# Optimization experiments

Measured on AMD Instinct MI355X. Metric: run time of the kernel, lower is better.

Reference implementation:

```python
import jax, jax.numpy as jnp
import numpy as np

NODE_DIM = 32
NUM_NODES = 256
BATCH = 32
HIDDEN = 64


def setup_inputs() -> dict:
    key = jax.random.key(0)
    k1, k2, k3, k4, k5 = jax.random.split(key, 5)
    node_features = jax.random.normal(k1, (BATCH, NUM_NODES, NODE_DIM), dtype=jnp.float32)
    # nn.Linear(node_dim*2, 64): weight [64, 2*node_dim], bias [64]
    s1 = 1.0 / np.sqrt(2 * NODE_DIM)
    W1 = jax.random.uniform(k2, (HIDDEN, 2 * NODE_DIM), minval=-s1, maxval=s1, dtype=jnp.float32)
    b1 = jax.random.uniform(k3, (HIDDEN,), minval=-s1, maxval=s1, dtype=jnp.float32)
    # nn.Linear(64, 1): weight [1, 64], bias [1]
    s2 = 1.0 / np.sqrt(HIDDEN)
    W2 = jax.random.uniform(k4, (1, HIDDEN), minval=-s2, maxval=s2, dtype=jnp.float32)
    b2 = jax.random.uniform(k5, (1,), minval=-s2, maxval=s2, dtype=jnp.float32)
    return {"node_features": node_features, "W1": W1, "b1": b1, "W2": W2, "b2": b2}


def reference(node_features, W1, b1, W2, b2):
    # fc1(concat(x_i, x_j)) splits as x_i @ W1a^T + x_j @ W1b^T (exact same math,
    # avoids materializing the [B,N,N,2d] pair tensor).
    d = node_features.shape[-1]
    W1a, W1b = W1[:, :d], W1[:, d:]
    Ai = jnp.einsum('bnd,hd->bnh', node_features, W1a)  # [B,N,H]
    Aj = jnp.einsum('bnd,hd->bnh', node_features, W1b)  # [B,N,H]
    hidden = jax.nn.relu(Ai[:, :, None, :] + Aj[:, None, :, :] + b1)  # [B,N,N,H]
    logits = jnp.einsum('bijh,h->bij', hidden, W2[0]) + b2[0]  # [B,N,N]
    return jax.nn.sigmoid(logits)
```

## Files before the change

### kernel.cpp

```cpp
#include <hip/hip_runtime.h>

typedef _Float16 h2 __attribute__((ext_vector_type(2)));
typedef _Float16 h8 __attribute__((ext_vector_type(8)));

#define BB 32
#define NN 256
#define DD 32
#define HH 64
#define ET 64
#define XST 40
#define AST 72

#if defined(__has_builtin)
#  if __has_builtin(__builtin_amdgcn_fdot2)
#    define FDOT2(a, b, c) __builtin_amdgcn_fdot2((a), (b), (c), false)
#  endif
#endif
#ifndef FDOT2
#  define FDOT2(a, b, c) ((c) + (float)((a)[0]) * (float)((b)[0]) + (float)((a)[1]) * (float)((b)[1]))
#endif

__device__ __forceinline__ float sigmoidf_fast(float v) {
    return 1.0f / (1.0f + __expf(-v));
}

__global__ __launch_bounds__(256) void fused_kernel(const float* __restrict__ x, const float* __restrict__ W1,
                                                    const float* __restrict__ b1, const float* __restrict__ W2,
                                                    const float* __restrict__ b2, float* __restrict__ out)
{
    __shared__ _Float16 sX[128][XST];
    __shared__ _Float16 sW[128][XST];
    __shared__ _Float16 sAi[ET][AST];
    __shared__ _Float16 sAj[ET][AST];
    __shared__ _Float16 sW2h[HH];

    const int blk = blockIdx.x;
    const int jt = blk & 3;
    const int it = (blk >> 2) & 3;
    const int b  = blk >> 4;
    const int tid = threadIdx.x;

    for (int k = tid; k < HH * 2 * DD; k += 256) {
        int h = k >> 6, c = k & 63;
        int hc = (c < 32) ? h : h + 64;
        int d  = c & 31;
        int phys = (hc >> 3) + ((hc & 7) << 4);
        sW[phys][d] = (_Float16)W1[k];
    }
    const float* xb = x + (size_t)b * NN * DD;
    for (int k = tid; k < 128 * DD; k += 256) {
        int row = k >> 5, d = k & 31;
        int grow = (row < 64) ? (it * ET + row) : (jt * ET + (row - 64));
        int phys = (row & 64) + ((row & 63) >> 2) + ((row & 3) << 4);
        sX[phys][d] = (_Float16)xb[(size_t)grow * DD + d];
    }
    if (tid < HH) sW2h[tid] = (_Float16)W2[tid];
    __syncthreads();

    {
        const int tcol = tid & 15;
        const int trow = tid >> 4;
        const int side = tcol >> 3;
        const int xbase = side * 64 + trow;
        const int h0 = (tcol & 7) * 8;

        float pacc[4][8] = {};
#pragma unroll
        for (int ch = 0; ch < 4; ++ch) {
            h8 xv[4], wv[8];
#pragma unroll
            for (int rr = 0; rr < 4; ++rr)
                xv[rr] = *(const h8*)&sX[xbase + 16 * rr][ch * 8];
#pragma unroll
            for (int cc = 0; cc < 8; ++cc)
                wv[cc] = *(const h8*)&sW[tcol + 16 * cc][ch * 8];
#pragma unroll
            for (int rr = 0; rr < 4; ++rr)
#pragma unroll
                for (int cc = 0; cc < 8; ++cc) {
                    float a = pacc[rr][cc];
                    a = FDOT2(__builtin_shufflevector(xv[rr], xv[rr], 0, 1),
                              __builtin_shufflevector(wv[cc], wv[cc], 0, 1), a);
                    a = FDOT2(__builtin_shufflevector(xv[rr], xv[rr], 2, 3),
                              __builtin_shufflevector(wv[cc], wv[cc], 2, 3), a);
                    a = FDOT2(__builtin_shufflevector(xv[rr], xv[rr], 4, 5),
                              __builtin_shufflevector(wv[cc], wv[cc], 4, 5), a);
                    a = FDOT2(__builtin_shufflevector(xv[rr], xv[rr], 6, 7),
                              __builtin_shufflevector(wv[cc], wv[cc], 6, 7), a);
                    pacc[rr][cc] = a;
                }
        }
        float badd[8];
#pragma unroll
        for (int cc = 0; cc < 8; ++cc) badd[cc] = (side == 0) ? 0.f : b1[h0 + cc];
        _Float16* dst = (side == 0) ? &sAi[0][0] : &sAj[0][0];
#pragma unroll
        for (int rr = 0; rr < 4; ++rr) {
            h8 v;
#pragma unroll
            for (int q = 0; q < 8; ++q) v[q] = (_Float16)(pacc[rr][q] + badd[q]);
            *(h8*)&dst[(size_t)(4 * trow + rr) * AST + h0] = v;
        }
    }
    __syncthreads();

    const int jl = tid & 15;
    const int il = tid >> 4;
    h8 w2v[8];
#pragma unroll
    for (int q = 0; q < 8; ++q) w2v[q] = *(const h8*)&sW2h[q * 8];

    float eacc[4][4] = {};
#pragma unroll
    for (int c8 = 0; c8 < 8; ++c8) {
        h8 av[4], cv[4];
#pragma unroll
        for (int r = 0; r < 4; ++r) av[r] = *(const h8*)&sAi[il + 16 * r][c8 * 8];
#pragma unroll
        for (int c = 0; c < 4; ++c) cv[c] = *(const h8*)&sAj[jl + 16 * c][c8 * 8];
#pragma unroll
        for (int r = 0; r < 4; ++r)
#pragma unroll
            for (int c = 0; c < 4; ++c) {
                h8 z  = av[r] + cv[c];
                h8 rl = __builtin_elementwise_max(z, (h8)(_Float16)0);
                float a = eacc[r][c];
                a = FDOT2(__builtin_shufflevector(rl, rl, 0, 1), __builtin_shufflevector(w2v[c8], w2v[c8], 0, 1), a);
                a = FDOT2(__builtin_shufflevector(rl, rl, 2, 3), __builtin_shufflevector(w2v[c8], w2v[c8], 2, 3), a);
                a = FDOT2(__builtin_shufflevector(rl, rl, 4, 5), __builtin_shufflevector(w2v[c8], w2v[c8], 4, 5), a);
                a = FDOT2(__builtin_shufflevector(rl, rl, 6, 7), __builtin_shufflevector(w2v[c8], w2v[c8], 6, 7), a);
                eacc[r][c] = a;
            }
    }

    const float b2v = b2[0];
    size_t base = ((size_t)b * NN + (size_t)it * ET + il) * NN + (size_t)jt * ET + jl;
#pragma unroll
    for (int r = 0; r < 4; ++r)
#pragma unroll
        for (int c = 0; c < 4; ++c)
            out[base + (size_t)(16 * r) * NN + 16 * c] = sigmoidf_fast(eacc[r][c] + b2v);
}

extern "C" void kernel_launch(void* const* d_in, const int* in_sizes, int n_in,
                              void* d_out, int out_size, void* d_ws, size_t ws_size,
                              hipStream_t stream) {
    const float* x  = (const float*)d_in[0];
    const float* W1 = (const float*)d_in[1];
    const float* b1 = (const float*)d_in[2];
    const float* W2 = (const float*)d_in[3];
    const float* b2 = (const float*)d_in[4];
    float* out = (float*)d_out;

    const int nTiles = BB * (NN / ET) * (NN / ET);
    fused_kernel<<<nTiles, 256, 0, stream>>>(x, W1, b1, W2, b2, out);
}
```

Before: 19.14 us.

## Enlarge output tile to 128x64 per block and vectorize staging loads

Each block now computes a 128x64 output tile instead of 64x64, halving the block count to 256, so the per-block W1 conversion and Aj projection are amortized over twice as many outputs. The prologue loads W1 and x as float4 and writes h8 vectors to shared memory, and b1 is staged in shared memory. The projection stage is split unevenly across waves: two waves compute the 128 Ai rows and two compute the 64 Aj rows. The cost is more registers per thread (32 accumulators in the pair stage, 64 in the Ai waves), fewer blocks on a GPU with many CUs, and load imbalance between the waves.

```diff
diff --git a/kernel.cpp b/kernel.cpp
--- a/kernel.cpp
+++ b/kernel.cpp
@@ -7,7 +7,8 @@
 #define NN 256
 #define DD 32
 #define HH 64
-#define ET 64
+#define ETI 128
+#define ETJ 64
 #define XST 40
 #define AST 72
 
@@ -28,78 +29,117 @@
                                                     const float* __restrict__ b1, const float* __restrict__ W2,
                                                     const float* __restrict__ b2, float* __restrict__ out)
 {
-    __shared__ _Float16 sX[128][XST];
+    __shared__ _Float16 sX[192][XST];
     __shared__ _Float16 sW[128][XST];
-    __shared__ _Float16 sAi[ET][AST];
-    __shared__ _Float16 sAj[ET][AST];
+    __shared__ _Float16 sAi[ETI][AST];
+    __shared__ _Float16 sAj[ETJ][AST];
     __shared__ _Float16 sW2h[HH];
+    __shared__ float sb1[HH];
 
     const int blk = blockIdx.x;
     const int jt = blk & 3;
-    const int it = (blk >> 2) & 3;
-    const int b  = blk >> 4;
+    const int it = (blk >> 2) & 1;
+    const int b  = blk >> 3;
     const int tid = threadIdx.x;
+    const float* xb = x + (size_t)b * NN * DD;
 
-    for (int k = tid; k < HH * 2 * DD; k += 256) {
-        int h = k >> 6, c = k & 63;
-        int hc = (c < 32) ? h : h + 64;
-        int d  = c & 31;
-        int phys = (hc >> 3) + ((hc & 7) << 4);
-        sW[phys][d] = (_Float16)W1[k];
+    {
+        const int hc = tid >> 1, d0 = (tid & 1) << 4;
+        const float* src = (hc < HH) ? &W1[hc * 64 + d0] : &W1[(hc - HH) * 64 + DD + d0];
+        float t16[16];
+        *(float4*)&t16[0]  = *(const float4*)&src[0];
+        *(float4*)&t16[4]  = *(const float4*)&src[4];
+        *(float4*)&t16[8]  = *(const float4*)&src[8];
+        *(float4*)&t16[12] = *(const float4*)&src[12];
+        const int phys = (hc >> 3) + ((hc & 7) << 4);
+        h8 v0, v1;
+#pragma unroll
+        for (int q = 0; q < 8; ++q) { v0[q] = (_Float16)t16[q]; v1[q] = (_Float16)t16[q + 8]; }
+        *(h8*)&sW[phys][d0]     = v0;
+        *(h8*)&sW[phys][d0 + 8] = v1;
     }
-    const float* xb = x + (size_t)b * NN * DD;
-    for (int k = tid; k < 128 * DD; k += 256) {
-        int row = k >> 5, d = k & 31;
-        int grow = (row < 64) ? (it * ET + row) : (jt * ET + (row - 64));
-        int phys = (row & 64) + ((row & 63) >> 2) + ((row & 3) << 4);
-        sX[phys][d] = (_Float16)xb[(size_t)grow * DD + d];
+    for (int k = tid; k < 384; k += 256) {
+        const int row = k >> 1, d0 = (k & 1) << 4;
+        int grow, phys;
+        if (row < 128) { grow = it * ETI + row; phys = (row >> 3) + ((row & 7) << 4); }
+        else { const int r = row - 128; grow = jt * ETJ + r; phys = 128 + (r >> 2) + ((r & 3) << 4); }
+        float t16[16];
+        const float* src = &xb[(size_t)grow * DD + d0];
+        *(float4*)&t16[0]  = *(const float4*)&src[0];
+        *(float4*)&t16[4]  = *(const float4*)&src[4];
+        *(float4*)&t16[8]  = *(const float4*)&src[8];
+        *(float4*)&t16[12] = *(const float4*)&src[12];
+        h8 v0, v1;
+#pragma unroll
+        for (int q = 0; q < 8; ++q) { v0[q] = (_Float16)t16[q]; v1[q] = (_Float16)t16[q + 8]; }
+        *(h8*)&sX[phys][d0]     = v0;
+        *(h8*)&sX[phys][d0 + 8] = v1;
     }
     if (tid < HH) sW2h[tid] = (_Float16)W2[tid];
+    else if (tid < 2 * HH) sb1[tid - HH] = b1[tid - HH];
     __syncthreads();
 
     {
-        const int tcol = tid & 15;
-        const int trow = tid >> 4;
-        const int side = tcol >> 3;
-        const int xbase = side * 64 + trow;
-        const int h0 = (tcol & 7) * 8;
-
-        float pacc[4][8] = {};
+        const int wid = tid >> 6, lane = tid & 63;
+        const int lq = lane >> 3, lp = lane & 7;
+        if (wid < 2) {
+            const int q = (wid << 3) | lq;
+            float pacc[8][8] = {};
 #pragma unroll
-        for (int ch = 0; ch < 4; ++ch) {
-            h8 xv[4], wv[8];
+            for (int ch = 0; ch < 4; ++ch) {
+                h8 xv[8], wv[8];
 #pragma unroll
-            for (int rr = 0; rr < 4; ++rr)
-                xv[rr] = *(const h8*)&sX[xbase + 16 * rr][ch * 8];
+                for (int rr = 0; rr < 8; ++rr) xv[rr] = *(const h8*)&sX[q + (rr << 4)][ch << 3];
 #pragma unroll
-            for (int cc = 0; cc < 8; ++cc)
-                wv[cc] = *(const h8*)&sW[tcol + 16 * cc][ch * 8];
+                for (int cc = 0; cc < 8; ++cc) wv[cc] = *(const h8*)&sW[lp + (cc << 4)][ch << 3];
 #pragma unroll
-            for (int rr = 0; rr < 4; ++rr)
+                for (int rr = 0; rr < 8; ++rr)
 #pragma unroll
-                for (int cc = 0; cc < 8; ++cc) {
-                    float a = pacc[rr][cc];
-                    a = FDOT2(__builtin_shufflevector(xv[rr], xv[rr], 0, 1),
-                              __builtin_shufflevector(wv[cc], wv[cc], 0, 1), a);
-                    a = FDOT2(__builtin_shufflevector(xv[rr], xv[rr], 2, 3),
-                              __builtin_shufflevector(wv[cc], wv[cc], 2, 3), a);
-                    a = FDOT2(__builtin_shufflevector(xv[rr], xv[rr], 4, 5),
-                              __builtin_shufflevector(wv[cc], wv[cc], 4, 5), a);
-                    a = FDOT2(__builtin_shufflevector(xv[rr], xv[rr], 6, 7),
-                              __builtin_shufflevector(wv[cc], wv[cc], 6, 7), a);
-                    pacc[rr][cc] = a;
-                }
-        }
-        float badd[8];
+                    for (int cc = 0; cc < 8; ++cc) {
+                        float a = pacc[rr][cc];
+                        a = FDOT2(__builtin_shufflevector(xv[rr], xv[rr], 0, 1), __builtin_shufflevector(wv[cc], wv[cc], 0, 1), a);
+                        a = FDOT2(__builtin_shufflevector(xv[rr], xv[rr], 2, 3), __builtin_shufflevector(wv[cc], wv[cc], 2, 3), a);
+                        a = FDOT2(__builtin_shufflevector(xv[rr], xv[rr], 4, 5), __builtin_shufflevector(wv[cc], wv[cc], 4, 5), a);
+                        a = FDOT2(__builtin_shufflevector(xv[rr], xv[rr], 6, 7), __builtin_shufflevector(wv[cc], wv[cc], 6, 7), a);
+                        pacc[rr][cc] = a;
+                    }
+            }
 #pragma unroll
-        for (int cc = 0; cc < 8; ++cc) badd[cc] = (side == 0) ? 0.f : b1[h0 + cc];
-        _Float16* dst = (side == 0) ? &sAi[0][0] : &sAj[0][0];
+            for (int rr = 0; rr < 8; ++rr) {
+                h8 v;
 #pragma unroll
-        for (int rr = 0; rr < 4; ++rr) {
-            h8 v;
+                for (int cc = 0; cc < 8; ++cc) v[cc] = (_Float16)pacc[rr][cc];
+                *(h8*)&sAi[(q << 3) | rr][lp << 3] = v;
+            }
+        } else {
+            const int wp = wid - 2;
+            float pacc[4][8] = {};
 #pragma unroll
-            for (int q = 0; q < 8; ++q) v[q] = (_Float16)(pacc[rr][q] + badd[q]);
-            *(h8*)&dst[(size_t)(4 * trow + rr) * AST + h0] = v;
+            for (int ch = 0; ch < 4; ++ch) {
+                h8 xv[4], wv[8];
+#pragma unroll
+                for (int rr = 0; rr < 4; ++rr) xv[rr] = *(const h8*)&sX[128 + (wp << 3) + lq + (rr << 4)][ch << 3];
+#pragma unroll
+                for (int cc = 0; cc < 8; ++cc) wv[cc] = *(const h8*)&sW[8 + lp + (cc << 4)][ch << 3];
+#pragma unroll
+                for (int rr = 0; rr < 4; ++rr)
+#pragma unroll
+                    for (int cc = 0; cc < 8; ++cc) {
+                        float a = pacc[rr][cc];
+                        a = FDOT2(__builtin_shufflevector(xv[rr], xv[rr], 0, 1), __builtin_shufflevector(wv[cc], wv[cc], 0, 1), a);
+                        a = FDOT2(__builtin_shufflevector(xv[rr], xv[rr], 2, 3), __builtin_shufflevector(wv[cc], wv[cc], 2, 3), a);
+                        a = FDOT2(__builtin_shufflevector(xv[rr], xv[rr], 4, 5), __builtin_shufflevector(wv[cc], wv[cc], 4, 5), a);
+                        a = FDOT2(__builtin_shufflevector(xv[rr], xv[rr], 6, 7), __builtin_shufflevector(wv[cc], wv[cc], 6, 7), a);
+                        pacc[rr][cc] = a;
+                    }
+            }
+#pragma unroll
+            for (int rr = 0; rr < 4; ++rr) {
+                h8 v;
+#pragma unroll
+                for (int cc = 0; cc < 8; ++cc) v[cc] = (_Float16)(pacc[rr][cc] + sb1[(lp << 3) + cc]);
+                *(h8*)&sAj[(wp << 5) + (lq << 2) + rr][lp << 3] = v;
+            }
         }
     }
     __syncthreads();
@@ -108,22 +148,22 @@
     const int il = tid >> 4;
     h8 w2v[8];
 #pragma unroll
-    for (int q = 0; q < 8; ++q) w2v[q] = *(const h8*)&sW2h[q * 8];
+    for (int q = 0; q < 8; ++q) w2v[q] = *(const h8*)&sW2h[q << 3];
 
-    float eacc[4][4] = {};
+    float eacc[8][4] = {};
 #pragma unroll
     for (int c8 = 0; c8 < 8; ++c8) {
-        h8 av[4], cv[4];
+        h8 av[8], cv[4];
 #pragma unroll
-        for (int r = 0; r < 4; ++r) av[r] = *(const h8*)&sAi[il + 16 * r][c8 * 8];
+        for (int r = 0; r < 8; ++r) av[r] = *(const h8*)&sAi[il + (r << 4)][c8 << 3];
 #pragma unroll
-        for (int c = 0; c < 4; ++c) cv[c] = *(const h8*)&sAj[jl + 16 * c][c8 * 8];
+        for (int c = 0; c < 4; ++c) cv[c] = *(const h8*)&sAj[jl + (c << 4)][c8 << 3];
 #pragma unroll
-        for (int r = 0; r < 4; ++r)
+        for (int r = 0; r < 8; ++r)
 #pragma unroll
             for (int c = 0; c < 4; ++c) {
                 h8 z  = av[r] + cv[c];
-                h8 rl = __builtin_elementwise_max(z, (h8)(_Float16)0);
+                h8 rl = __builtin_elementwise_max(z, h8{});
                 float a = eacc[r][c];
                 a = FDOT2(__builtin_shufflevector(rl, rl, 0, 1), __builtin_shufflevector(w2v[c8], w2v[c8], 0, 1), a);
                 a = FDOT2(__builtin_shufflevector(rl, rl, 2, 3), __builtin_shufflevector(w2v[c8], w2v[c8], 2, 3), a);
@@ -134,12 +174,12 @@
     }
 
     const float b2v = b2[0];
-    size_t base = ((size_t)b * NN + (size_t)it * ET + il) * NN + (size_t)jt * ET + jl;
+    const size_t base = (((size_t)(b * NN) + it * ETI + il) << 8) + jt * ETJ + jl;
 #pragma unroll
-    for (int r = 0; r < 4; ++r)
+    for (int r = 0; r < 8; ++r)
 #pragma unroll
         for (int c = 0; c < 4; ++c)
-            out[base + (size_t)(16 * r) * NN + 16 * c] = sigmoidf_fast(eacc[r][c] + b2v);
+            out[base + (size_t)(r << 4) * NN + (c << 4)] = sigmoidf_fast(eacc[r][c] + b2v);
 }
 
 extern "C" void kernel_launch(void* const* d_in, const int* in_sizes, int n_in,
@@ -152,6 +192,6 @@
     const float* b2 = (const float*)d_in[4];
     float* out = (float*)d_out;
 
-    const int nTiles = BB * (NN / ET) * (NN / ET);
-    fused_kernel<<<nTiles, 256, 0, stream>>>(x, W1, b1, W2, b2, out);
+    const int nBlocks = BB * (NN / ETI) * (NN / ETJ);
+    fused_kernel<<<nBlocks, 256, 0, stream>>>(x, W1, b1, W2, b2, out);
 }
```

Measured after the change: 17.99 us. 6.0% less time.
